# Kernel tuning notes

Measured on AMD Instinct MI355X. Metric: run time of the kernel, lower is better.

Reference implementation:

```python
import jax, jax.numpy as jnp
import numpy as np

EMBED_DIM = 1024
NUM_HEADS = 16
GQA = 4
KV_HEADS = NUM_HEADS // GQA          # 4
HEAD_DIM = EMBED_DIM // NUM_HEADS    # 64
KV_EMBED = KV_HEADS * HEAD_DIM       # 512
EPS = 1e-3
B, T = 2, 1024


def monotonic_attention(probs):
    """Many-to-many monotonic attention over sigmoid probs.

    probs: (..., Tq, Tk) in (0,1).
    Recurrence: phi[0] = onehot(key 0);
      phi[i, j] = p[i-1, j] * phi[i-1, j] + (1 - p[i, j-1]) * phi[i, j-1].
    The inner (j) recurrence is a first-order linear recurrence solved with
    an associative scan; the outer (i) recurrence uses lax.scan.
    """
    p = jnp.clip(probs, EPS, 1.0 - EPS)
    p_t = jnp.moveaxis(p, -2, 0)  # (Tq, ..., Tk)
    init = jnp.zeros(p_t.shape[1:], p.dtype).at[..., 0].set(1.0)

    def combine(x, y):
        A1, b1 = x
        A2, b2 = y
        return (A1 * A2, b1 * A2 + b2)

    def step(phi_prev, rows):
        p_prev, p_cur = rows
        a = phi_prev * p_prev                    # mass arriving from row above
        q = 1.0 - p_cur                          # stay-in-row (move right) prob
        A = jnp.concatenate([jnp.zeros_like(q[..., :1]), q[..., :-1]], axis=-1)
        _, phi = jax.lax.associative_scan(combine, (A, a), axis=-1)
        return phi, phi

    _, phis = jax.lax.scan(step, init, (p_t[:-1], p_t[1:]))
    phis = jnp.concatenate([init[None], phis], axis=0)  # (Tq, ..., Tk)
    return jnp.moveaxis(phis, 0, -2)


def setup_inputs() -> dict:
    key = jax.random.key(0)
    ks = jax.random.split(key, 5)
    scale_in = (2.0 / (EMBED_DIM + 2 * KV_EMBED + EMBED_DIM)) ** 0.5  # xavier-ish
    scale_out = (2.0 / (2 * EMBED_DIM)) ** 0.5
    return {
        "query": jax.random.normal(ks[0], (B, T, EMBED_DIM), jnp.float32),
        "key": jax.random.normal(ks[1], (B, T, EMBED_DIM), jnp.float32),
        "value": jax.random.normal(ks[2], (B, T, EMBED_DIM), jnp.float32),
        "in_proj_weight": jax.random.normal(ks[3], (EMBED_DIM + 2 * KV_EMBED, EMBED_DIM), jnp.float32) * scale_in,
        "in_proj_bias": jnp.zeros((EMBED_DIM + 2 * KV_EMBED,), jnp.float32),
        "out_proj_weight": jax.random.normal(ks[4], (EMBED_DIM, EMBED_DIM), jnp.float32) * scale_out,
        "out_proj_bias": jnp.zeros((EMBED_DIM,), jnp.float32),
    }


def reference(query, key, value, in_proj_weight, in_proj_bias, out_proj_weight, out_proj_bias):
    qw = in_proj_weight[:EMBED_DIM]
    kw = in_proj_weight[EMBED_DIM:EMBED_DIM + KV_EMBED]
    vw = in_proj_weight[EMBED_DIM + KV_EMBED:]
    qb = in_proj_bias[:EMBED_DIM]
    kb = in_proj_bias[EMBED_DIM:EMBED_DIM + KV_EMBED]
    vb = in_proj_bias[EMBED_DIM + KV_EMBED:]

    b, tq, _ = query.shape
    tk = key.shape[1]
    xq = query @ qw.T + qb   # (B, Tq, E)
    xk = key @ kw.T + kb     # (B, Tk, KV_EMBED)
    xv = value @ vw.T + vb   # (B, Tk, KV_EMBED)

    # (B, G, H, Tq, C) and (B, H, Tk, C)
    xq = xq.reshape(b, tq, GQA, KV_HEADS, HEAD_DIM).transpose(0, 2, 3, 1, 4)
    xk = xk.reshape(b, tk, KV_HEADS, HEAD_DIM).transpose(0, 2, 1, 3)
    xv = xv.reshape(b, tk, KV_HEADS, HEAD_DIM).transpose(0, 2, 1, 3)

    attn = jnp.einsum("bghqc,bhkc->bghqk", xq, xk)
    attn = monotonic_attention(jax.nn.sigmoid(attn))
    xo = jnp.einsum("bghqk,bhkc->bghqc", attn, xv)
    xo = xo.transpose(0, 3, 1, 2, 4).reshape(b, tq, EMBED_DIM)
    return xo @ out_proj_weight.T + out_proj_bias
```

## Files before the change

kernel.cpp:

```cpp
#include <hip/hip_runtime.h>
#include <cstddef>
#include <cstdint>

#define TSEQ 1024

typedef __attribute__((ext_vector_type(8))) short short8;
typedef __attribute__((ext_vector_type(4))) float floatx4;

static constexpr size_t OFF_XQ  = 0;
static constexpr size_t OFF_XK  = (size_t)2 * 1024 * 1024;
static constexpr size_t OFF_XVT = OFF_XK + (size_t)512 * 1024;
static constexpr size_t OFF_XO  = OFF_XVT + (size_t)512 * 1024;
static constexpr size_t OFF_P   = OFF_XO + (size_t)2 * 1024 * 1024;


__device__ __forceinline__ void cvt_hi_lo(float x, unsigned short& hi,
                                          unsigned short& lo) {
  unsigned u = __float_as_uint(x);
  unsigned rh = (u + 0x7FFFu + ((u >> 16) & 1u)) & 0xFFFF0000u;
  hi = (unsigned short)(rh >> 16);
  float xl = x - __uint_as_float(rh);
  unsigned ul = __float_as_uint(xl);
  unsigned rl = ul + 0x7FFFu + ((ul >> 16) & 1u);
  lo = (unsigned short)(rl >> 16);
}

__device__ __forceinline__ int diagrow(int r, int cblk) {
  return ((((r >> 2) + cblk) & 255) << 2) | (r & 3);
}

template <int EPI, int ADIAG, int CDIAG>
__device__ __forceinline__ void mfma_nt_core(
    const float* __restrict__ A, int lda,
    const float* __restrict__ B, int ldb,
    float* __restrict__ C, int ldc, int K,
    const float* __restrict__ bias)
{
  __shared__ __align__(16) unsigned short Ah[64][40];
  __shared__ __align__(16) unsigned short Al[64][40];
  __shared__ __align__(16) unsigned short Bh[64][40];
  __shared__ __align__(16) unsigned short Bl[64][40];

  const int bm = blockIdx.y << 6;
  const int bn = blockIdx.x << 6;
  const int tid  = threadIdx.x;
  const int lane = tid & 63;
  const int wave = tid >> 6;
  const int m16  = lane & 15;
  const int quad = lane >> 4;

  const int srow = tid >> 2;
  const int skq  = (tid & 3) << 3;

  floatx4 acc[4];
#pragma unroll
  for (int c = 0; c < 4; ++c) acc[c] = (floatx4){0.f, 0.f, 0.f, 0.f};

  for (int k0 = 0; k0 < K; k0 += 32) {
    {
      const int kq = k0 + skq;
      int arow = bm + srow;
      if (ADIAG) arow = diagrow(arow, kq >> 4);
      const float* ap = A + (size_t)arow * lda + kq;
      const float* bp = B + (size_t)(bn + srow) * ldb + kq;
      float av[8] __attribute__((aligned(16)));
      float bv[8] __attribute__((aligned(16)));
      *(float4*)&av[0] = *(const float4*)(ap);
      *(float4*)&av[4] = *(const float4*)(ap + 4);
      *(float4*)&bv[0] = *(const float4*)(bp);
      *(float4*)&bv[4] = *(const float4*)(bp + 4);
      short8 vah, valo, vbh, vblo;
#pragma unroll
      for (int e = 0; e < 8; ++e) {
        unsigned short h, l;
        cvt_hi_lo(av[e], h, l);
        vah[e] = (short)h; valo[e] = (short)l;
        cvt_hi_lo(bv[e], h, l);
        vbh[e] = (short)h; vblo[e] = (short)l;
      }
      *(short8*)&Ah[srow][skq] = vah;
      *(short8*)&Al[srow][skq] = valo;
      *(short8*)&Bh[srow][skq] = vbh;
      *(short8*)&Bl[srow][skq] = vblo;
    }
    __syncthreads();

    const int arow = (wave << 4) + m16;
    const short8 a_h = *(const short8*)&Ah[arow][quad << 3];
    const short8 a_l = *(const short8*)&Al[arow][quad << 3];
#pragma unroll
    for (int c = 0; c < 4; ++c) {
      const int brow = (c << 4) + m16;
      const short8 b_h = *(const short8*)&Bh[brow][quad << 3];
      const short8 b_l = *(const short8*)&Bl[brow][quad << 3];
      acc[c] = __builtin_amdgcn_mfma_f32_16x16x32_bf16(a_h, b_h, acc[c], 0, 0, 0);
      acc[c] = __builtin_amdgcn_mfma_f32_16x16x32_bf16(a_h, b_l, acc[c], 0, 0, 0);
      acc[c] = __builtin_amdgcn_mfma_f32_16x16x32_bf16(a_l, b_h, acc[c], 0, 0, 0);
    }
    __syncthreads();
  }

#pragma unroll
  for (int c = 0; c < 4; ++c) {
#pragma unroll
    for (int r = 0; r < 4; ++r) {
      const int row = (wave << 4) + (quad << 2) + r;
      const int col = (c << 4) + m16;
      float v = acc[c][r];
      if (EPI == 0) { if (bias) v += bias[bn + col]; }
      if (EPI == 1) { v += bias[bm + row]; }
      if (EPI == 2) {
        v = 1.0f / (1.0f + expf(v));
        v = fminf(fmaxf(v, 0.001f), 0.999f);
      }
      int crow = bm + row;
      if (CDIAG) crow = diagrow(crow, (bn + col) >> 4);
      C[(size_t)crow * ldc + (bn + col)] = v;
    }
  }
}

__global__ __launch_bounds__(256) void gemm_nt_mfma_k(
    const float* __restrict__ A, int lda, const float* __restrict__ W, int ldw,
    const float* __restrict__ bias, float* __restrict__ C, int ldc, int K)
{
  mfma_nt_core<0, 0, 0>(A, lda, W, ldw, C, ldc, K, bias);
}

__global__ __launch_bounds__(256) void proj_vt_k(
    const float* __restrict__ vw, const float* __restrict__ value,
    const float* __restrict__ vb, float* __restrict__ XVt)
{
  const int b = blockIdx.z;
  mfma_nt_core<1, 0, 0>(vw, 1024, value + ((size_t)b << 20), 1024,
                        XVt + (size_t)b * 256 * 1024, 1024, 1024, vb);
}

__global__ __launch_bounds__(256) void scores_mfma_k(
    const float* __restrict__ XQ, const float* __restrict__ XK,
    float* __restrict__ P)
{
  const int z = blockIdx.z;
  const int b = z >> 4;
  mfma_nt_core<2, 0, 1>(XQ + ((size_t)b << 20) + ((size_t)(z & 15) << 6), 1024,
                        XK + (size_t)b * TSEQ * 256 + ((size_t)(z & 3) << 6), 256,
                        P + ((size_t)z << 20), 1024, 64, nullptr);
}

__global__ __launch_bounds__(256) void pv_mfma_k(
    const float* __restrict__ P, const float* __restrict__ XVt,
    float* __restrict__ XO)
{
  const int z = blockIdx.z;
  const int b = z >> 4;
  mfma_nt_core<0, 1, 0>(P + ((size_t)z << 20), 1024,
                        XVt + (size_t)b * 256 * 1024 + (size_t)(z & 3) * 64 * 1024, 1024,
                        XO + ((size_t)b << 20) + ((size_t)(z & 15) << 6), 1024,
                        1024, nullptr);
}

__global__ __launch_bounds__(64) void mono_rec_k(float* __restrict__ P)
{
  const int z = blockIdx.x;
  float* __restrict__ Pz = P + ((size_t)z << 20);
  const int t = threadIdx.x;
  const int col0 = t << 4;

  float b[16];
#pragma unroll
  for (int c = 0; c < 16; ++c) b[c] = 0.0f;
  float phi15h[4], q15h[4];
#pragma unroll
  for (int k = 0; k < 4; ++k) { phi15h[k] = 0.0f; q15h[k] = 0.0f; }

  float pA[4][16], pB[4][16];

#pragma unroll
  for (int k = 0; k < 4; ++k) {
    const float* lp = Pz + (k << 10) + col0;
#pragma unroll
    for (int q = 0; q < 4; ++q)
      *(float4*)&pA[k][4 * q] = *(const float4*)(lp + 4 * q);
  }

  auto step = [&](int s, float (&pcur)[4][16], float (&pnext)[4][16]) {
    float phiL[4], qL[4];
#pragma unroll
    for (int k = 0; k < 4; ++k) {
      phiL[k] = __shfl_up(phi15h[k], 1);
      qL[k]   = __shfl_up(q15h[k], 1);
    }

    {
      const float* np = Pz + ((size_t)((s + 1) & 255) << 12) + col0;
#pragma unroll
      for (int k = 0; k < 4; ++k)
#pragma unroll
        for (int q = 0; q < 4; ++q)
          *(float4*)&pnext[k][4 * q] = *(const float4*)(np + (k << 10) + 4 * q);
    }

    const int g = s - t;
    if (g >= 0 && g < 256) {
      float* sp = Pz + ((size_t)(s & 255) << 12) + col0;
      float phi[16];
#pragma unroll
      for (int k = 0; k < 4; ++k) {
        const float* qk = pcur[k];
        if (g == 0 && k == 0) {
#pragma unroll
          for (int c = 0; c < 16; ++c) phi[c] = 0.0f;
          if (t == 0) phi[0] = 1.0f;
        } else {
          const float H0 = (t == 0) ? 0.0f : qL[k];
          float x = fmaf(H0, phiL[k], b[0]);
          phi[0] = x;
#pragma unroll
          for (int c = 1; c < 16; ++c) {
            x = fmaf(qk[c - 1], x, b[c]);
            phi[c] = x;
          }
        }
#pragma unroll
        for (int c = 0; c < 16; ++c) b[c] = fmaf(-qk[c], phi[c], phi[c]);
        q15h[k]   = qk[15];
        phi15h[k] = phi[15];
#pragma unroll
        for (int q = 0; q < 4; ++q)
          *(float4*)(sp + (k << 10) + 4 * q) = *(float4*)&phi[4 * q];
      }
    }
  };

  for (int s0 = 0; s0 < 320; s0 += 2) {
    step(s0, pA, pB);
    step(s0 + 1, pB, pA);
  }
}

extern "C" void kernel_launch(void* const* d_in, const int* in_sizes, int n_in,
                              void* d_out, int out_size, void* d_ws, size_t ws_size,
                              hipStream_t stream)
{
  const float* query = (const float*)d_in[0];
  const float* key   = (const float*)d_in[1];
  const float* value = (const float*)d_in[2];
  const float* ipw   = (const float*)d_in[3];
  const float* ipb   = (const float*)d_in[4];
  const float* opw   = (const float*)d_in[5];
  const float* opb   = (const float*)d_in[6];
  float* out = (float*)d_out;
  float* ws  = (float*)d_ws;

  float* XQ  = ws + OFF_XQ;
  float* XK  = ws + OFF_XK;
  float* XVt = ws + OFF_XVT;
  float* XO  = ws + OFF_XO;
  float* P   = ws + OFF_P;

  gemm_nt_mfma_k<<<dim3(16, 32), 256, 0, stream>>>(
      query, 1024, ipw, 1024, ipb, XQ, 1024, 1024);
  gemm_nt_mfma_k<<<dim3(4, 32), 256, 0, stream>>>(
      key, 1024, ipw + (size_t)1024 * 1024, 1024, ipb + 1024, XK, 256, 1024);
  proj_vt_k<<<dim3(16, 4, 2), 256, 0, stream>>>(
      ipw + (size_t)1280 * 1024, value, ipb + 1280, XVt);

  scores_mfma_k<<<dim3(16, 16, 32), 256, 0, stream>>>(XQ, XK, P);

  mono_rec_k<<<dim3(32), dim3(64), 0, stream>>>(P);

  pv_mfma_k<<<dim3(1, 16, 32), 256, 0, stream>>>(P, XVt, XO);

  gemm_nt_mfma_k<<<dim3(16, 32), 256, 0, stream>>>(
      XO, 1024, opw, 1024, opb, out, 1024, 1024);
}
```

Baseline: 555.5 us.

## Split monotonic recurrence into compute wave plus helper waves staging rows via LDS

The recurrence kernel now runs 320 threads per block. One wavefront does the serial wavefront computation and reads p values from shared memory. Four helper wavefronts prefetch upcoming rows from global memory, transpose them into a shared-memory ring of four slots, and write finished phi rows from a double-buffered LDS area back to global with coalesced float4 stores. This takes global load latency and uncoalesced strided accesses off the serial critical path. In exchange it adds two block-wide barriers per step and about 96KB of LDS.

```diff
diff --git a/kernel.cpp b/kernel.cpp
--- a/kernel.cpp
+++ b/kernel.cpp
@@ -159,12 +159,16 @@
                         1024, nullptr);
 }
 
-__global__ __launch_bounds__(64) void mono_rec_k(float* __restrict__ P)
+__global__ __launch_bounds__(320, 1) void mono_rec_k(float* __restrict__ P)
 {
   const int z = blockIdx.x;
   float* __restrict__ Pz = P + ((size_t)z << 20);
-  const int t = threadIdx.x;
-  const int col0 = t << 4;
+  const int tid = threadIdx.x;
+  const int w   = tid >> 6;
+  const int l   = tid & 63;
+
+  __shared__ __align__(16) float Qs[4 * 4096];
+  __shared__ __align__(16) float Pb[2 * 4096];
 
   float b[16];
 #pragma unroll
@@ -173,68 +177,110 @@
 #pragma unroll
   for (int k = 0; k < 4; ++k) { phi15h[k] = 0.0f; q15h[k] = 0.0f; }
 
-  float pA[4][16], pB[4][16];
-
-#pragma unroll
-  for (int k = 0; k < 4; ++k) {
-    const float* lp = Pz + (k << 10) + col0;
-#pragma unroll
-    for (int q = 0; q < 4; ++q)
-      *(float4*)&pA[k][4 * q] = *(const float4*)(lp + 4 * q);
+  float4 bufA[4], bufB[4];
+
+  if (w > 0) {
+    const int k = w - 1;
+    float4 t0[4];
+    const float* g0 = Pz + (k << 10) + (l << 2);
+#pragma unroll
+    for (int m = 0; m < 4; ++m) t0[m] = *(const float4*)(g0 + (m << 8));
+    const int base = (k << 10) + ((l & 3) << 8) + ((l >> 2) << 1);
+#pragma unroll
+    for (int m = 0; m < 4; ++m) {
+      *(float2*)&Qs[base + (m << 5)]       = make_float2(t0[m].x, t0[m].y);
+      *(float2*)&Qs[base + (m << 5) + 128] = make_float2(t0[m].z, t0[m].w);
+    }
+    const float* g1 = Pz + (1 << 12) + (k << 10) + (l << 2);
+#pragma unroll
+    for (int m = 0; m < 4; ++m) bufB[m] = *(const float4*)(g1 + (m << 8));
   }
-
-  auto step = [&](int s, float (&pcur)[4][16], float (&pnext)[4][16]) {
+  __syncthreads();
+
+  auto cstep = [&](int s) {
+    const int rb = (s & 3) << 12;
+    float q[4][16];
+#pragma unroll
+    for (int k = 0; k < 4; ++k)
+#pragma unroll
+      for (int j = 0; j < 8; ++j) {
+        float2 v = *(const float2*)&Qs[rb + (k << 10) + (j << 7) + (l << 1)];
+        q[k][2 * j]     = v.x;
+        q[k][2 * j + 1] = v.y;
+      }
     float phiL[4], qL[4];
 #pragma unroll
     for (int k = 0; k < 4; ++k) {
       phiL[k] = __shfl_up(phi15h[k], 1);
       qL[k]   = __shfl_up(q15h[k], 1);
     }
-
-    {
-      const float* np = Pz + ((size_t)((s + 1) & 255) << 12) + col0;
-#pragma unroll
-      for (int k = 0; k < 4; ++k)
-#pragma unroll
-        for (int q = 0; q < 4; ++q)
-          *(float4*)&pnext[k][4 * q] = *(const float4*)(np + (k << 10) + 4 * q);
-    }
-
-    const int g = s - t;
+    const int g = s - l;
     if (g >= 0 && g < 256) {
-      float* sp = Pz + ((size_t)(s & 255) << 12) + col0;
-      float phi[16];
+      const int pbb = (s & 1) << 12;
 #pragma unroll
       for (int k = 0; k < 4; ++k) {
-        const float* qk = pcur[k];
+        float phi[16];
         if (g == 0 && k == 0) {
 #pragma unroll
           for (int c = 0; c < 16; ++c) phi[c] = 0.0f;
-          if (t == 0) phi[0] = 1.0f;
+          if (l == 0) phi[0] = 1.0f;
         } else {
-          const float H0 = (t == 0) ? 0.0f : qL[k];
+          const float H0 = (l == 0) ? 0.0f : qL[k];
           float x = fmaf(H0, phiL[k], b[0]);
           phi[0] = x;
 #pragma unroll
           for (int c = 1; c < 16; ++c) {
-            x = fmaf(qk[c - 1], x, b[c]);
+            x = fmaf(q[k][c - 1], x, b[c]);
             phi[c] = x;
           }
         }
 #pragma unroll
-        for (int c = 0; c < 16; ++c) b[c] = fmaf(-qk[c], phi[c], phi[c]);
-        q15h[k]   = qk[15];
+        for (int c = 0; c < 16; ++c) b[c] = fmaf(-q[k][c], phi[c], phi[c]);
+        q15h[k]   = q[k][15];
         phi15h[k] = phi[15];
 #pragma unroll
-        for (int q = 0; q < 4; ++q)
-          *(float4*)(sp + (k << 10) + 4 * q) = *(float4*)&phi[4 * q];
+        for (int j = 0; j < 8; ++j)
+          *(float2*)&Pb[pbb + (k << 10) + (j << 7) + (l << 1)] =
+              make_float2(phi[2 * j], phi[2 * j + 1]);
       }
     }
   };
 
+  auto hstep = [&](int s, float4 (&ld)[4], const float4 (&wr)[4]) {
+    const int k = w - 1;
+    const float* gp = Pz + ((size_t)((s + 2) & 255) << 12) + (k << 10) + (l << 2);
+#pragma unroll
+    for (int m = 0; m < 4; ++m) ld[m] = *(const float4*)(gp + (m << 8));
+    {
+      const int base = (((s + 1) & 3) << 12) + (k << 10) +
+                       ((l & 3) << 8) + ((l >> 2) << 1);
+#pragma unroll
+      for (int m = 0; m < 4; ++m) {
+        *(float2*)&Qs[base + (m << 5)]       = make_float2(wr[m].x, wr[m].y);
+        *(float2*)&Qs[base + (m << 5) + 128] = make_float2(wr[m].z, wr[m].w);
+      }
+    }
+    if (s > 0) {
+      const int sf = s - 1;
+      const int rbase = ((sf & 1) << 12) + (k << 10) +
+                        ((l & 3) << 8) + ((l >> 2) << 1);
+      float* sp = Pz + ((size_t)(sf & 255) << 12) + (k << 10) + (l << 2);
+#pragma unroll
+      for (int m = 0; m < 4; ++m) {
+        float2 a = *(const float2*)&Pb[rbase + (m << 5)];
+        float2 c = *(const float2*)&Pb[rbase + (m << 5) + 128];
+        const int T = (m << 4) + (l >> 2);
+        if (T <= sf && T >= sf - 255)
+          *(float4*)(sp + (m << 8)) = make_float4(a.x, a.y, c.x, c.y);
+      }
+    }
+  };
+
   for (int s0 = 0; s0 < 320; s0 += 2) {
-    step(s0, pA, pB);
-    step(s0 + 1, pB, pA);
+    if (w == 0) cstep(s0); else hstep(s0, bufA, bufB);
+    __syncthreads();
+    if (w == 0) cstep(s0 + 1); else hstep(s0 + 1, bufB, bufA);
+    __syncthreads();
   }
 }
 
@@ -267,7 +313,7 @@
 
   scores_mfma_k<<<dim3(16, 16, 32), 256, 0, stream>>>(XQ, XK, P);
 
-  mono_rec_k<<<dim3(32), dim3(64), 0, stream>>>(P);
+  mono_rec_k<<<dim3(32), dim3(320), 0, stream>>>(P);
 
   pv_mfma_k<<<dim3(1, 16, 32), 256, 0, stream>>>(P, XVt, XO);
 
```

Measured after the change: 608.8 us. 9.6% more time.

## Warp-specialize monotonic recurrence with helper waves staging loads/stores through LDS

Applied to the files above, without the earlier changes.

The single-wave recurrence kernel becomes a 320-thread block: wave 0 runs the serial wavefront recurrence, and four helper waves prefetch upcoming P tiles into LDS (transposed) and write computed phi tiles from LDS back to global memory. This takes global load latency and store traffic off the critical serial path. It costs a block barrier per step plus LDS traffic, and only 32 blocks still run.

```diff
diff --git a/kernel.cpp b/kernel.cpp
--- a/kernel.cpp
+++ b/kernel.cpp
@@ -159,31 +159,76 @@
                         1024, nullptr);
 }
 
-__global__ __launch_bounds__(64) void mono_rec_k(float* __restrict__ P)
+#define MONO_BAR() do {                                          \
+    asm volatile("s_waitcnt lgkmcnt(0)" ::: "memory");           \
+    __builtin_amdgcn_sched_barrier(0);                           \
+    asm volatile("s_barrier" ::: "memory");                      \
+    __builtin_amdgcn_sched_barrier(0);                           \
+  } while (0)
+
+__global__ __launch_bounds__(320, 1) void mono_rec_k(float* __restrict__ P)
 {
   const int z = blockIdx.x;
   float* __restrict__ Pz = P + ((size_t)z << 20);
-  const int t = threadIdx.x;
-  const int col0 = t << 4;
+  const int tid = threadIdx.x;
+  const int w   = tid >> 6;
+  const int l   = tid & 63;
+
+  __shared__ float Qr[2][4][16][64];
+  __shared__ float Pr[2][4][16][64];
 
   float b[16];
+  float phi15h[4], q15h[4];
 #pragma unroll
   for (int c = 0; c < 16; ++c) b[c] = 0.0f;
-  float phi15h[4], q15h[4];
 #pragma unroll
   for (int k = 0; k < 4; ++k) { phi15h[k] = 0.0f; q15h[k] = 0.0f; }
 
-  float pA[4][16], pB[4][16];
-
-#pragma unroll
-  for (int k = 0; k < 4; ++k) {
-    const float* lp = Pz + (k << 10) + col0;
-#pragma unroll
-    for (int q = 0; q < 4; ++q)
-      *(float4*)&pA[k][4 * q] = *(const float4*)(lp + 4 * q);
-  }
-
-  auto step = [&](int s, float (&pcur)[4][16], float (&pnext)[4][16]) {
+  const int hk = (w > 0) ? (w - 1) : 0;
+  float4 bufX[4], bufY[4];
+
+  auto hload = [&](int slot, float4 (&buf)[4]) {
+    const float* gp = Pz + ((size_t)(slot & 255) << 12) + (hk << 10) + (l << 2);
+#pragma unroll
+    for (int m = 0; m < 4; ++m) buf[m] = *(const float4*)(gp + (m << 8));
+  };
+  auto hpub = [&](int s1, const float4 (&buf)[4]) {
+    const int rb = s1 & 1;
+    const int j0 = (l & 3) << 2;
+#pragma unroll
+    for (int m = 0; m < 4; ++m) {
+      const int tt = (m << 4) + (l >> 2);
+      Qr[rb][hk][j0 + 0][tt] = buf[m].x;
+      Qr[rb][hk][j0 + 1][tt] = buf[m].y;
+      Qr[rb][hk][j0 + 2][tt] = buf[m].z;
+      Qr[rb][hk][j0 + 3][tt] = buf[m].w;
+    }
+  };
+  auto hflush = [&](int sf) {
+    const int rb = sf & 1;
+    const int j0 = (l & 3) << 2;
+    float* sp = Pz + ((size_t)(sf & 255) << 12) + (hk << 10) + (l << 2);
+#pragma unroll
+    for (int m = 0; m < 4; ++m) {
+      const int T = (m << 4) + (l >> 2);
+      if (T <= sf && T >= sf - 255) {
+        float4 v = make_float4(Pr[rb][hk][j0 + 0][T],
+                               Pr[rb][hk][j0 + 1][T],
+                               Pr[rb][hk][j0 + 2][T],
+                               Pr[rb][hk][j0 + 3][T]);
+        *(float4*)(sp + (m << 8)) = v;
+      }
+    }
+  };
+
+  auto cstep = [&](int s) {
+    const int rb = s & 1;
+    float q[4][16];
+#pragma unroll
+    for (int k = 0; k < 4; ++k)
+#pragma unroll
+      for (int j = 0; j < 16; ++j) q[k][j] = Qr[rb][k][j][l];
+
     float phiL[4], qL[4];
 #pragma unroll
     for (int k = 0; k < 4; ++k) {
@@ -191,50 +236,57 @@
       qL[k]   = __shfl_up(q15h[k], 1);
     }
 
-    {
-      const float* np = Pz + ((size_t)((s + 1) & 255) << 12) + col0;
-#pragma unroll
-      for (int k = 0; k < 4; ++k)
-#pragma unroll
-        for (int q = 0; q < 4; ++q)
-          *(float4*)&pnext[k][4 * q] = *(const float4*)(np + (k << 10) + 4 * q);
-    }
-
-    const int g = s - t;
+    const int g = s - l;
     if (g >= 0 && g < 256) {
-      float* sp = Pz + ((size_t)(s & 255) << 12) + col0;
-      float phi[16];
 #pragma unroll
       for (int k = 0; k < 4; ++k) {
-        const float* qk = pcur[k];
+        float phi[16];
         if (g == 0 && k == 0) {
 #pragma unroll
           for (int c = 0; c < 16; ++c) phi[c] = 0.0f;
-          if (t == 0) phi[0] = 1.0f;
+          if (l == 0) phi[0] = 1.0f;
         } else {
-          const float H0 = (t == 0) ? 0.0f : qL[k];
+          const float H0 = (l == 0) ? 0.0f : qL[k];
           float x = fmaf(H0, phiL[k], b[0]);
           phi[0] = x;
 #pragma unroll
           for (int c = 1; c < 16; ++c) {
-            x = fmaf(qk[c - 1], x, b[c]);
+            x = fmaf(q[k][c - 1], x, b[c]);
             phi[c] = x;
           }
         }
 #pragma unroll
-        for (int c = 0; c < 16; ++c) b[c] = fmaf(-qk[c], phi[c], phi[c]);
-        q15h[k]   = qk[15];
+        for (int c = 0; c < 16; ++c) b[c] = fmaf(-q[k][c], phi[c], phi[c]);
+        q15h[k]   = q[k][15];
         phi15h[k] = phi[15];
 #pragma unroll
-        for (int q = 0; q < 4; ++q)
-          *(float4*)(sp + (k << 10) + 4 * q) = *(float4*)&phi[4 * q];
+        for (int j = 0; j < 16; ++j) Pr[rb][k][j][l] = phi[j];
       }
     }
   };
 
-  for (int s0 = 0; s0 < 320; s0 += 2) {
-    step(s0, pA, pB);
-    step(s0 + 1, pB, pA);
+  if (w > 0) {
+    hload(0, bufX);
+    hload(1, bufY);
+    hpub(0, bufX);
+  }
+  MONO_BAR();
+
+  if (w == 0) cstep(0);
+  else { hload(2, bufX); hpub(1, bufY); }
+  MONO_BAR();
+
+  if (w == 0) cstep(1);
+  else { hload(3, bufY); hpub(2, bufX); hflush(0); }
+  MONO_BAR();
+
+  for (int s = 2; s < 320; s += 2) {
+    if (w == 0) cstep(s);
+    else { hload(s + 2, bufX); hpub(s + 1, bufY); hflush(s - 1); }
+    MONO_BAR();
+    if (w == 0) cstep(s + 1);
+    else { hload(s + 3, bufY); hpub(s + 2, bufX); hflush(s); }
+    MONO_BAR();
   }
 }
 
@@ -267,7 +319,7 @@
 
   scores_mfma_k<<<dim3(16, 16, 32), 256, 0, stream>>>(XQ, XK, P);
 
-  mono_rec_k<<<dim3(32), dim3(64), 0, stream>>>(P);
+  mono_rec_k<<<dim3(32), dim3(320), 0, stream>>>(P);
 
   pv_mfma_k<<<dim3(1, 16, 32), 256, 0, stream>>>(P, XVt, XO);
 
```

New measurement: 596.5 us. 7.4% more time.
